# Kernel optimization log

Measured on AMD Instinct MI355X. Metric: run time of the kernel, lower is better.

The kernel has to match this reference:

```python
import jax, jax.numpy as jnp
import numpy as np


def setup_inputs() -> dict:
    key = jax.random.key(0)
    ks = jax.random.split(key, 7)
    B, T, Fin, H, O = 32, 2048, 256, 256, 256
    s = 1.0 / np.sqrt(H)
    return {
        "x":   jax.random.normal(ks[0], (B, T, Fin), dtype=jnp.float32),
        "h0":  jax.random.normal(ks[1], (B, H), dtype=jnp.float32),
        "Wxh": jax.random.normal(ks[2], (H, Fin), dtype=jnp.float32) * s,
        "bxh": jax.random.normal(ks[3], (H,), dtype=jnp.float32) * s,
        "Whh": jax.random.normal(ks[4], (H, H), dtype=jnp.float32) * s,
        "Why": jax.random.normal(ks[5], (O, H), dtype=jnp.float32) * s,
        "by":  jax.random.normal(ks[6], (O,), dtype=jnp.float32) * s,
    }


def reference(x, h0, Wxh, bxh, Whh, Why, by):
    # Batch the input projection across all T as one GEMM: (B,T,Fin)x(Fin,H)
    xh = jnp.einsum('btf,hf->bth', x, Wxh) + bxh  # (B,T,H)

    def step(h, xh_t):
        h = jnp.tanh(xh_t + h @ Whh.T)  # (B,H)
        return h, h

    # scan over time (axis 0 after transpose)
    h_final, hs = jax.lax.scan(step, h0, jnp.swapaxes(xh, 0, 1))  # hs: (T,B,H)
    hs = jnp.swapaxes(hs, 0, 1)  # (B,T,H)
    # Batch the output projection across all T as one GEMM
    y = jnp.einsum('bth,oh->bto', hs, Why) + by  # (B,T,O)
    return (y, h_final)
```

## Files before the change

kernel.cpp:

```cpp
#include <hip/hip_runtime.h>
#include <hip/hip_bf16.h>
#include <hip/hip_fp16.h>


typedef _Float16 f16x8 __attribute__((ext_vector_type(8)));
typedef float    f32x4 __attribute__((ext_vector_type(4)));

#define MFMA16 __builtin_amdgcn_mfma_f32_16x16x32_f16

__device__ __forceinline__ f16x8 cvt8(const float* __restrict__ p) {
    float4 u = *(const float4*)p;
    float4 v = *(const float4*)(p + 4);
    f16x8 r;
    r[0] = (_Float16)u.x; r[1] = (_Float16)u.y; r[2] = (_Float16)u.z; r[3] = (_Float16)u.w;
    r[4] = (_Float16)v.x; r[5] = (_Float16)v.y; r[6] = (_Float16)v.z; r[7] = (_Float16)v.w;
    return r;
}

template<bool AF16>
__global__ __launch_bounds__(256, 2) void gemm_nt_256(
    const void* __restrict__ Av, const float* __restrict__ W,
    const float* __restrict__ bias, float* __restrict__ C) {
    const int tid = threadIdx.x;
    const int l  = tid & 63;
    const int w  = tid >> 6;
    const int lr = l & 15;
    const int lg = l >> 4;
    const long m0 = (long)blockIdx.x * 64;
    const int  n0 = w * 64;

    f32x4 acc[4][4] = {};

    #pragma unroll
    for (int k = 0; k < 8; ++k) {
        const int kc = k * 32 + lg * 8;
        f16x8 a[4], bf[4];
        #pragma unroll
        for (int mt = 0; mt < 4; ++mt) {
            const long row = m0 + mt * 16 + lr;
            if constexpr (AF16)
                a[mt] = *(const f16x8*)((const _Float16*)Av + row * 256 + kc);
            else
                a[mt] = cvt8((const float*)Av + row * 256 + kc);
        }
        #pragma unroll
        for (int nt = 0; nt < 4; ++nt)
            bf[nt] = cvt8(W + (long)(n0 + nt * 16 + lr) * 256 + kc);
        #pragma unroll
        for (int mt = 0; mt < 4; ++mt)
            #pragma unroll
            for (int nt = 0; nt < 4; ++nt)
                acc[mt][nt] = MFMA16(a[mt], bf[nt], acc[mt][nt], 0, 0, 0);
    }

    #pragma unroll
    for (int mt = 0; mt < 4; ++mt)
        #pragma unroll
        for (int nt = 0; nt < 4; ++nt) {
            const int col = n0 + nt * 16 + lr;
            const float bv = bias[col];
            #pragma unroll
            for (int d = 0; d < 4; ++d) {
                const long row = m0 + mt * 16 + lg * 4 + d;
                C[row * 256 + col] = acc[mt][nt][d] + bv;
            }
        }
}

__global__ __launch_bounds__(512, 1) void rnn_scan(
    const float* __restrict__ xh, const float* __restrict__ h0,
    const float* __restrict__ Whh, _Float16* __restrict__ hs,
    float* __restrict__ hfin) {
    const int b   = blockIdx.x;
    const int tid = threadIdx.x;
    const int l   = tid & 63;
    const int w   = tid >> 6;
    const int lr  = l & 15;
    const int lg  = l >> 4;
    const int n0  = w * 32;

    __shared__ _Float16 hbuf[2][256];

    f16x8 wb[2][8];
    #pragma unroll
    for (int nt = 0; nt < 2; ++nt)
        #pragma unroll
        for (int k = 0; k < 8; ++k)
            wb[nt][k] = cvt8(Whh + (long)(n0 + nt * 16 + lr) * 256 + k * 32 + lg * 8);

    if (tid < 256) hbuf[0][tid] = (_Float16)h0[b * 256 + tid];
    __syncthreads();

    const int cl = n0 + (l & 31);
    const float* xp = xh + (long)b * 2048 * 256 + cl;
    _Float16*    hp = hs + (long)b * 2048 * 256 + cl;

    float xcur[4], xnext[4];
    #pragma unroll
    for (int j = 0; j < 4; ++j) xcur[j] = xp[(long)j * 256];

    for (int tb = 0; tb < 2048; tb += 4) {
        #pragma unroll
        for (int j = 0; j < 4; ++j) {
            long tn = tb + 4 + j; if (tn > 2047) tn = 2047;
            xnext[j] = xp[tn * 256];
        }

        #pragma unroll
        for (int j = 0; j < 4; ++j) {
            const f16x8* hc = (const f16x8*)hbuf[j & 1];
            f16x8 af[8];
            #pragma unroll
            for (int k = 0; k < 8; ++k) af[k] = hc[k * 4 + lg];
            __builtin_amdgcn_sched_barrier(0);

            const f32x4 zero = {0.f, 0.f, 0.f, 0.f};
            f32x4 accA[2], accB[2];
            #pragma unroll
            for (int nt = 0; nt < 2; ++nt) {
                accA[nt] = MFMA16(af[0], wb[nt][0], zero, 0, 0, 0);
                accB[nt] = MFMA16(af[4], wb[nt][4], zero, 0, 0, 0);
            }
            #pragma unroll
            for (int k = 1; k < 4; ++k)
                #pragma unroll
                for (int nt = 0; nt < 2; ++nt) {
                    accA[nt] = MFMA16(af[k],     wb[nt][k],     accA[nt], 0, 0, 0);
                    accB[nt] = MFMA16(af[k + 4], wb[nt][k + 4], accB[nt], 0, 0, 0);
                }

            const float s0 = accA[0][0] + accB[0][0];
            const float s1 = accA[1][0] + accB[1][0];
            const float s  = ((l & 16) ? s1 : s0) + xcur[j];
            const float e  = __expf(2.0f * s);
            const float v  = 1.0f - 2.0f * __builtin_amdgcn_rcpf(e + 1.0f);
            const _Float16 hv = (_Float16)v;

            if (l < 32) {
                hbuf[(j & 1) ^ 1][cl] = hv;
                hp[(long)(tb + j) * 256] = hv;
            }

            asm volatile("s_waitcnt lgkmcnt(0)" ::: "memory");
            __builtin_amdgcn_s_barrier();
            asm volatile("" ::: "memory");
        }

        #pragma unroll
        for (int j = 0; j < 4; ++j) xcur[j] = xnext[j];
    }

    if (tid < 256) hfin[b * 256 + tid] = (float)hbuf[0][tid];
}

extern "C" void kernel_launch(void* const* d_in, const int* in_sizes, int n_in,
                              void* d_out, int out_size, void* d_ws, size_t ws_size,
                              hipStream_t stream) {
    const float* x   = (const float*)d_in[0];
    const float* h0  = (const float*)d_in[1];
    const float* Wxh = (const float*)d_in[2];
    const float* bxh = (const float*)d_in[3];
    const float* Whh = (const float*)d_in[4];
    const float* Why = (const float*)d_in[5];
    const float* by  = (const float*)d_in[6];

    float* y    = (float*)d_out;
    float* hfin = y + (long)65536 * 256;
    float* xh   = y;
    _Float16* hs = (_Float16*)d_ws;

    gemm_nt_256<false><<<1024, 256, 0, stream>>>(x, Wxh, bxh, xh);
    rnn_scan<<<32, 512, 0, stream>>>(xh, h0, Whh, hs, hfin);
    gemm_nt_256<true><<<1024, 256, 0, stream>>>(hs, Why, by, y);
}
```

Before: 935.2 us.

## Replace per-step workgroup barrier with LDS flag spin-wait in RNN scan

The scan kernel no longer ends each timestep with s_barrier. Instead, each wave publishes its new slice of h to a double-buffered LDS array and raises a per-wave flag. Before reading the other slices, it spins on the eight flags using a ballot. Each wave's K order is rotated so it starts the MFMA on its own h slice before waiting, overlapping part of the serial recurrence with synchronisation. The cost is active spinning on volatile LDS reads, and correctness now depends on flag and buffer ordering rather than a hardware barrier.

Measured after the change: 1.112 ms. +18.9%, slower.

```diff
diff --git a/kernel.cpp b/kernel.cpp
--- a/kernel.cpp
+++ b/kernel.cpp
@@ -80,20 +80,26 @@
     const int n0  = w * 32;
 
     __shared__ _Float16 hbuf[2][256];
+    __shared__ unsigned flags[8];
 
-    f16x8 wb[2][8];
+    f16x8 wbr[2][8];
     #pragma unroll
-    for (int nt = 0; nt < 2; ++nt)
+    for (int i = 0; i < 8; ++i) {
+        const int k = (w + i) & 7;
         #pragma unroll
-        for (int k = 0; k < 8; ++k)
-            wb[nt][k] = cvt8(Whh + (long)(n0 + nt * 16 + lr) * 256 + k * 32 + lg * 8);
+        for (int nt = 0; nt < 2; ++nt)
+            wbr[nt][i] = cvt8(Whh + (long)(n0 + nt * 16 + lr) * 256 + k * 32 + lg * 8);
+    }
 
-    if (tid < 256) hbuf[0][tid] = (_Float16)h0[b * 256 + tid];
+    if (tid < 8) flags[tid] = 0;
     __syncthreads();
 
     const int cl = n0 + (l & 31);
     const float* xp = xh + (long)b * 2048 * 256 + cl;
     _Float16*    hp = hs + (long)b * 2048 * 256 + cl;
+    volatile unsigned* fl = flags;
+
+    _Float16 hv = (_Float16)h0[b * 256 + cl];
 
     float xcur[4], xnext[4];
     #pragma unroll
@@ -108,49 +114,54 @@
 
         #pragma unroll
         for (int j = 0; j < 4; ++j) {
-            const f16x8* hc = (const f16x8*)hbuf[j & 1];
-            f16x8 af[8];
-            #pragma unroll
-            for (int k = 0; k < 8; ++k) af[k] = hc[k * 4 + lg];
-            __builtin_amdgcn_sched_barrier(0);
+            const int t = tb + j;
+            _Float16* hb = hbuf[j & 1];
+            const f16x8* hc = (const f16x8*)hb;
+
+            if (l < 32) hb[cl] = hv;
+            asm volatile("s_waitcnt lgkmcnt(0)" ::: "memory");
+            if (l == 0) fl[w] = (unsigned)(t + 1);
+
+            f16x8 afr[8];
+            afr[0] = hc[(w & 7) * 4 + lg];
 
             const f32x4 zero = {0.f, 0.f, 0.f, 0.f};
             f32x4 accA[2], accB[2];
+            accA[0] = MFMA16(afr[0], wbr[0][0], zero, 0, 0, 0);
+            accA[1] = MFMA16(afr[0], wbr[1][0], zero, 0, 0, 0);
+
+            unsigned fv;
+            do { fv = fl[l & 7]; } while (__ballot(fv > (unsigned)t) != ~0ull);
+
             #pragma unroll
-            for (int nt = 0; nt < 2; ++nt) {
-                accA[nt] = MFMA16(af[0], wb[nt][0], zero, 0, 0, 0);
-                accB[nt] = MFMA16(af[4], wb[nt][4], zero, 0, 0, 0);
+            for (int i = 1; i < 8; ++i)
+                afr[i] = hc[((w + i) & 7) * 4 + lg];
+
+            accB[0] = MFMA16(afr[1], wbr[0][1], zero, 0, 0, 0);
+            accB[1] = MFMA16(afr[1], wbr[1][1], zero, 0, 0, 0);
+            #pragma unroll
+            for (int i = 2; i < 8; i += 2) {
+                accA[0] = MFMA16(afr[i],     wbr[0][i],     accA[0], 0, 0, 0);
+                accA[1] = MFMA16(afr[i],     wbr[1][i],     accA[1], 0, 0, 0);
+                accB[0] = MFMA16(afr[i + 1], wbr[0][i + 1], accB[0], 0, 0, 0);
+                accB[1] = MFMA16(afr[i + 1], wbr[1][i + 1], accB[1], 0, 0, 0);
             }
-            #pragma unroll
-            for (int k = 1; k < 4; ++k)
-                #pragma unroll
-                for (int nt = 0; nt < 2; ++nt) {
-                    accA[nt] = MFMA16(af[k],     wb[nt][k],     accA[nt], 0, 0, 0);
-                    accB[nt] = MFMA16(af[k + 4], wb[nt][k + 4], accB[nt], 0, 0, 0);
-                }
 
             const float s0 = accA[0][0] + accB[0][0];
             const float s1 = accA[1][0] + accB[1][0];
             const float s  = ((l & 16) ? s1 : s0) + xcur[j];
             const float e  = __expf(2.0f * s);
             const float v  = 1.0f - 2.0f * __builtin_amdgcn_rcpf(e + 1.0f);
-            const _Float16 hv = (_Float16)v;
+            hv = (_Float16)v;
 
-            if (l < 32) {
-                hbuf[(j & 1) ^ 1][cl] = hv;
-                hp[(long)(tb + j) * 256] = hv;
-            }
-
-            asm volatile("s_waitcnt lgkmcnt(0)" ::: "memory");
-            __builtin_amdgcn_s_barrier();
-            asm volatile("" ::: "memory");
+            if (l < 32) hp[(long)t * 256] = hv;
         }
 
         #pragma unroll
         for (int j = 0; j < 4; ++j) xcur[j] = xnext[j];
     }
 
-    if (tid < 256) hfin[b * 256 + tid] = (float)hbuf[0][tid];
+    if (l < 32) hfin[b * 256 + cl] = (float)hv;
 }
 
 extern "C" void kernel_launch(void* const* d_in, const int* in_sizes, int n_in,
```

## Replace MFMA recurrent matvec with per-lane scalar FMA dot products

Applied to the files above, without the earlier changes.

The recurrent step h@Whh^T in the scan kernel now uses plain FP32 FMAs instead of 16x16x32 MFMA tiles. Each lane holds half of one Whh row (128 fp16 values) in registers, reads the matching half of h from shared memory, and the two halves are combined with a cross-lane shuffle. The goal is to shorten the serial per-timestep latency: the old version ran a chain of dependent MFMAs per step and kept only one column of each 16x16 result. In exchange each lane does 128 scalar FMAs with fp16-to-fp32 conversions and reads 256 bytes of h from LDS per step. The final hidden state is now written in fp32 at the last step instead of being read back from the fp16 buffer.

Result: slower. 1.720 ms (+83.9%).

```diff
diff --git a/kernel.cpp b/kernel.cpp
--- a/kernel.cpp
+++ b/kernel.cpp
@@ -3,8 +3,8 @@
 #include <hip/hip_fp16.h>
 
 
-typedef _Float16 f16x8 __attribute__((ext_vector_type(8)));
-typedef float    f32x4 __attribute__((ext_vector_type(4)));
+typedef _Float16 f16x8  __attribute__((ext_vector_type(8)));
+typedef float    f32x4  __attribute__((ext_vector_type(4)));
 
 #define MFMA16 __builtin_amdgcn_mfma_f32_16x16x32_f16
 
@@ -71,29 +71,27 @@
     const float* __restrict__ xh, const float* __restrict__ h0,
     const float* __restrict__ Whh, _Float16* __restrict__ hs,
     float* __restrict__ hfin) {
-    const int b   = blockIdx.x;
-    const int tid = threadIdx.x;
-    const int l   = tid & 63;
-    const int w   = tid >> 6;
-    const int lr  = l & 15;
-    const int lg  = l >> 4;
-    const int n0  = w * 32;
+    const int b    = blockIdx.x;
+    const int tid  = threadIdx.x;
+    const int l    = tid & 63;
+    const int w    = tid >> 6;
+    const int col  = w * 32 + (l & 31);
+    const int half = l >> 5;
 
     __shared__ _Float16 hbuf[2][256];
 
-    f16x8 wb[2][8];
-    #pragma unroll
-    for (int nt = 0; nt < 2; ++nt)
+    f16x8 wreg8[16];
+    {
+        const float* wp = Whh + (long)col * 256 + half * 128;
         #pragma unroll
-        for (int k = 0; k < 8; ++k)
-            wb[nt][k] = cvt8(Whh + (long)(n0 + nt * 16 + lr) * 256 + k * 32 + lg * 8);
+        for (int i = 0; i < 16; ++i) wreg8[i] = cvt8(wp + 8 * i);
+    }
 
     if (tid < 256) hbuf[0][tid] = (_Float16)h0[b * 256 + tid];
     __syncthreads();
 
-    const int cl = n0 + (l & 31);
-    const float* xp = xh + (long)b * 2048 * 256 + cl;
-    _Float16*    hp = hs + (long)b * 2048 * 256 + cl;
+    const float* xp = xh + (long)b * 2048 * 256 + col;
+    _Float16*    hp = hs + (long)b * 2048 * 256 + col;
 
     float xcur[4], xnext[4];
     #pragma unroll
@@ -108,37 +106,40 @@
 
         #pragma unroll
         for (int j = 0; j < 4; ++j) {
-            const f16x8* hc = (const f16x8*)hbuf[j & 1];
-            f16x8 af[8];
+            const int t = tb + j;
+
+            const f16x8* hc = (const f16x8*)hbuf[j & 1] + half * 16;
+            f16x8 hreg[16];
             #pragma unroll
-            for (int k = 0; k < 8; ++k) af[k] = hc[k * 4 + lg];
-            __builtin_amdgcn_sched_barrier(0);
+            for (int i = 0; i < 16; ++i) hreg[i] = hc[i];
 
-            const f32x4 zero = {0.f, 0.f, 0.f, 0.f};
-            f32x4 accA[2], accB[2];
+            float s0 = 0.f, s1 = 0.f, s2 = 0.f, s3 = 0.f;
             #pragma unroll
-            for (int nt = 0; nt < 2; ++nt) {
-                accA[nt] = MFMA16(af[0], wb[nt][0], zero, 0, 0, 0);
-                accB[nt] = MFMA16(af[4], wb[nt][4], zero, 0, 0, 0);
+            for (int i = 0; i < 16; ++i) {
+                const f16x8 h8 = hreg[i];
+                const f16x8 w8 = wreg8[i];
+                s0 = fmaf((float)h8[0], (float)w8[0], s0);
+                s0 = fmaf((float)h8[1], (float)w8[1], s0);
+                s1 = fmaf((float)h8[2], (float)w8[2], s1);
+                s1 = fmaf((float)h8[3], (float)w8[3], s1);
+                s2 = fmaf((float)h8[4], (float)w8[4], s2);
+                s2 = fmaf((float)h8[5], (float)w8[5], s2);
+                s3 = fmaf((float)h8[6], (float)w8[6], s3);
+                s3 = fmaf((float)h8[7], (float)w8[7], s3);
             }
-            #pragma unroll
-            for (int k = 1; k < 4; ++k)
-                #pragma unroll
-                for (int nt = 0; nt < 2; ++nt) {
-                    accA[nt] = MFMA16(af[k],     wb[nt][k],     accA[nt], 0, 0, 0);
-                    accB[nt] = MFMA16(af[k + 4], wb[nt][k + 4], accB[nt], 0, 0, 0);
-                }
+            float s = (s0 + s1) + (s2 + s3);
 
-            const float s0 = accA[0][0] + accB[0][0];
-            const float s1 = accA[1][0] + accB[1][0];
-            const float s  = ((l & 16) ? s1 : s0) + xcur[j];
-            const float e  = __expf(2.0f * s);
+            s += __shfl_xor(s, 32, 64);
+
+            const float sx = s + xcur[j];
+            const float e  = __expf(2.0f * sx);
             const float v  = 1.0f - 2.0f * __builtin_amdgcn_rcpf(e + 1.0f);
             const _Float16 hv = (_Float16)v;
 
             if (l < 32) {
-                hbuf[(j & 1) ^ 1][cl] = hv;
-                hp[(long)(tb + j) * 256] = hv;
+                hbuf[(j & 1) ^ 1][col] = hv;
+                hp[(long)t * 256] = hv;
+                if (t == 2047) hfin[b * 256 + col] = v;
             }
 
             asm volatile("s_waitcnt lgkmcnt(0)" ::: "memory");
@@ -149,8 +150,6 @@
         #pragma unroll
         for (int j = 0; j < 4; ++j) xcur[j] = xnext[j];
     }
-
-    if (tid < 256) hfin[b * 256 + tid] = (float)hbuf[0][tid];
 }
 
 extern "C" void kernel_launch(void* const* d_in, const int* in_sizes, int n_in,
```

## Fuse input projection, recurrent scan and output projection into one kernel

Applied to the files above, without the earlier changes.

Replaces the three launches (input GEMM, scan, output GEMM) with a single 32-block kernel, one block per batch. Each block first computes its own input projection with Wxh held in registers. During the latency-bound scan it then interleaves output-projection MFMAs for 16-timestep tiles, lagging the recurrence by 8 tiles, and finishes the last tiles after the loop. The aim is to remove the separate GEMM launches and hide the output GEMM inside idle scan cycles. The cost is a serial prologue that now runs on only 32 CUs, with every wave re-reading the batch's x slab, plus extra register pressure during the scan.

Result: slower. 1.604 ms (+71.5%).

```diff
diff --git a/kernel.cpp b/kernel.cpp
--- a/kernel.cpp
+++ b/kernel.cpp
@@ -1,5 +1,4 @@
 #include <hip/hip_runtime.h>
-#include <hip/hip_bf16.h>
 #include <hip/hip_fp16.h>
 
 
@@ -17,60 +16,14 @@
     return r;
 }
 
-template<bool AF16>
-__global__ __launch_bounds__(256, 2) void gemm_nt_256(
-    const void* __restrict__ Av, const float* __restrict__ W,
-    const float* __restrict__ bias, float* __restrict__ C) {
-    const int tid = threadIdx.x;
-    const int l  = tid & 63;
-    const int w  = tid >> 6;
-    const int lr = l & 15;
-    const int lg = l >> 4;
-    const long m0 = (long)blockIdx.x * 64;
-    const int  n0 = w * 64;
-
-    f32x4 acc[4][4] = {};
-
-    #pragma unroll
-    for (int k = 0; k < 8; ++k) {
-        const int kc = k * 32 + lg * 8;
-        f16x8 a[4], bf[4];
-        #pragma unroll
-        for (int mt = 0; mt < 4; ++mt) {
-            const long row = m0 + mt * 16 + lr;
-            if constexpr (AF16)
-                a[mt] = *(const f16x8*)((const _Float16*)Av + row * 256 + kc);
-            else
-                a[mt] = cvt8((const float*)Av + row * 256 + kc);
-        }
-        #pragma unroll
-        for (int nt = 0; nt < 4; ++nt)
-            bf[nt] = cvt8(W + (long)(n0 + nt * 16 + lr) * 256 + kc);
-        #pragma unroll
-        for (int mt = 0; mt < 4; ++mt)
-            #pragma unroll
-            for (int nt = 0; nt < 4; ++nt)
-                acc[mt][nt] = MFMA16(a[mt], bf[nt], acc[mt][nt], 0, 0, 0);
-    }
-
-    #pragma unroll
-    for (int mt = 0; mt < 4; ++mt)
-        #pragma unroll
-        for (int nt = 0; nt < 4; ++nt) {
-            const int col = n0 + nt * 16 + lr;
-            const float bv = bias[col];
-            #pragma unroll
-            for (int d = 0; d < 4; ++d) {
-                const long row = m0 + mt * 16 + lg * 4 + d;
-                C[row * 256 + col] = acc[mt][nt][d] + bv;
-            }
-        }
-}
-
-__global__ __launch_bounds__(512, 1) void rnn_scan(
-    const float* __restrict__ xh, const float* __restrict__ h0,
-    const float* __restrict__ Whh, _Float16* __restrict__ hs,
-    float* __restrict__ hfin) {
+__global__ __launch_bounds__(512, 1) void rnn_fused(
+    const float* __restrict__ x,   const float* __restrict__ h0,
+    const float* __restrict__ Wxh, const float* __restrict__ bxh,
+    const float* __restrict__ Whh, const float* __restrict__ Why,
+    const float* __restrict__ by,
+    float* __restrict__ xy,
+    float* __restrict__ hfin,
+    _Float16* __restrict__ hs) {
     const int b   = blockIdx.x;
     const int tid = threadIdx.x;
     const int l   = tid & 63;
@@ -78,8 +31,13 @@
     const int lr  = l & 15;
     const int lg  = l >> 4;
     const int n0  = w * 32;
+    const int cl  = n0 + (l & 31);
 
     __shared__ _Float16 hbuf[2][256];
+
+    const float* xb  = x  + (long)b * 2048 * 256;
+    float*       xyb = xy + (long)b * 2048 * 256;
+    _Float16*    hpB = hs + (long)b * 2048 * 256;
 
     f16x8 wb[2][8];
     #pragma unroll
@@ -88,18 +46,78 @@
         for (int k = 0; k < 8; ++k)
             wb[nt][k] = cvt8(Whh + (long)(n0 + nt * 16 + lr) * 256 + k * 32 + lg * 8);
 
+    f16x8 wg[2][8];
+    #pragma unroll
+    for (int nt = 0; nt < 2; ++nt)
+        #pragma unroll
+        for (int k = 0; k < 8; ++k)
+            wg[nt][k] = cvt8(Wxh + (long)(n0 + nt * 16 + lr) * 256 + k * 32 + lg * 8);
+
     if (tid < 256) hbuf[0][tid] = (_Float16)h0[b * 256 + tid];
+
+    for (int mt = 0; mt < 128; ++mt) {
+        f32x4 ac[2] = {{0.f,0.f,0.f,0.f},{0.f,0.f,0.f,0.f}};
+        #pragma unroll
+        for (int k = 0; k < 8; ++k) {
+            const int kc = k * 32 + lg * 8;
+            f16x8 a = cvt8(xb + (long)(mt * 16 + lr) * 256 + kc);
+            ac[0] = MFMA16(a, wg[0][k], ac[0], 0, 0, 0);
+            ac[1] = MFMA16(a, wg[1][k], ac[1], 0, 0, 0);
+        }
+        #pragma unroll
+        for (int nt = 0; nt < 2; ++nt) {
+            const int col = n0 + nt * 16 + lr;
+            const float bv = bxh[col];
+            #pragma unroll
+            for (int d = 0; d < 4; ++d)
+                xyb[(long)(mt * 16 + lg * 4 + d) * 256 + col] = ac[nt][d] + bv;
+        }
+    }
+
+    #pragma unroll
+    for (int nt = 0; nt < 2; ++nt)
+        #pragma unroll
+        for (int k = 0; k < 8; ++k)
+            wg[nt][k] = cvt8(Why + (long)(n0 + nt * 16 + lr) * 256 + k * 32 + lg * 8);
+
     __syncthreads();
 
-    const int cl = n0 + (l & 31);
-    const float* xp = xh + (long)b * 2048 * 256 + cl;
-    _Float16*    hp = hs + (long)b * 2048 * 256 + cl;
+    const float* xp = xyb + cl;
+    _Float16*    hp = hpB + cl;
 
     float xcur[4], xnext[4];
     #pragma unroll
     for (int j = 0; j < 4; ++j) xcur[j] = xp[(long)j * 256];
 
+    f32x4 sacc[2] = {{0.f,0.f,0.f,0.f},{0.f,0.f,0.f,0.f}};
+    f16x8 pya[4];
+
+#define YS(P, K)                                               \
+    do {                                                       \
+        sacc[0] = MFMA16(pya[P], wg[0][K], sacc[0], 0, 0, 0);  \
+        sacc[1] = MFMA16(pya[P], wg[1][K], sacc[1], 0, 0, 0);  \
+    } while (0)
+
     for (int tb = 0; tb < 2048; tb += 4) {
+        const int g = tb >> 4;
+        const int m = g - 8;
+        const bool yact = (m >= 0) && (m <= 118);
+
+        if (yact && (tb & 15) == 0) {
+            const _Float16* ap = hpB + (long)(m * 16 + lr) * 256 + lg * 8;
+            pya[0] = *(const f16x8*)(ap);
+            pya[1] = *(const f16x8*)(ap + 32);
+            pya[2] = *(const f16x8*)(ap + 64);
+            pya[3] = *(const f16x8*)(ap + 96);
+        }
+        if (yact && (tb & 15) == 8) {
+            const _Float16* ap = hpB + (long)(m * 16 + lr) * 256 + 128 + lg * 8;
+            pya[0] = *(const f16x8*)(ap);
+            pya[1] = *(const f16x8*)(ap + 32);
+            pya[2] = *(const f16x8*)(ap + 64);
+            pya[3] = *(const f16x8*)(ap + 96);
+        }
+
         #pragma unroll
         for (int j = 0; j < 4; ++j) {
             long tn = tb + 4 + j; if (tn > 2047) tn = 2047;
@@ -108,6 +126,7 @@
 
         #pragma unroll
         for (int j = 0; j < 4; ++j) {
+            const int t = tb + j;
             const f16x8* hc = (const f16x8*)hbuf[j & 1];
             f16x8 af[8];
             #pragma unroll
@@ -138,7 +157,25 @@
 
             if (l < 32) {
                 hbuf[(j & 1) ^ 1][cl] = hv;
-                hp[(long)(tb + j) * 256] = hv;
+                hp[(long)t * 256] = hv;
+                if (t == 2047) hfin[b * 256 + cl] = v;
+            }
+
+            if (j == 1 && yact) {
+                switch ((tb >> 2) & 3) {
+                    case 0: YS(0, 0); break;
+                    case 1: YS(2, 2); break;
+                    case 2: YS(0, 4); break;
+                    case 3: YS(2, 6); break;
+                }
+            }
+            if (j == 3 && yact) {
+                switch ((tb >> 2) & 3) {
+                    case 0: YS(1, 1); break;
+                    case 1: YS(3, 3); break;
+                    case 2: YS(1, 5); break;
+                    case 3: YS(3, 7); break;
+                }
             }
 
             asm volatile("s_waitcnt lgkmcnt(0)" ::: "memory");
@@ -146,11 +183,42 @@
             asm volatile("" ::: "memory");
         }
 
+        if (yact && (tb & 15) == 12) {
+            #pragma unroll
+            for (int nt = 0; nt < 2; ++nt) {
+                const int col = n0 + nt * 16 + lr;
+                const float bv = by[col];
+                #pragma unroll
+                for (int d = 0; d < 4; ++d)
+                    xyb[(long)(m * 16 + lg * 4 + d) * 256 + col] = sacc[nt][d] + bv;
+                sacc[nt] = (f32x4){0.f, 0.f, 0.f, 0.f};
+            }
+        }
+
         #pragma unroll
         for (int j = 0; j < 4; ++j) xcur[j] = xnext[j];
     }
 
-    if (tid < 256) hfin[b * 256 + tid] = (float)hbuf[0][tid];
+    __syncthreads();
+    for (int mt = 119; mt < 128; ++mt) {
+        f32x4 ac[2] = {{0.f,0.f,0.f,0.f},{0.f,0.f,0.f,0.f}};
+        #pragma unroll
+        for (int k = 0; k < 8; ++k) {
+            const int kc = k * 32 + lg * 8;
+            f16x8 a = *(const f16x8*)(hpB + (long)(mt * 16 + lr) * 256 + kc);
+            ac[0] = MFMA16(a, wg[0][k], ac[0], 0, 0, 0);
+            ac[1] = MFMA16(a, wg[1][k], ac[1], 0, 0, 0);
+        }
+        #pragma unroll
+        for (int nt = 0; nt < 2; ++nt) {
+            const int col = n0 + nt * 16 + lr;
+            const float bv = by[col];
+            #pragma unroll
+            for (int d = 0; d < 4; ++d)
+                xyb[(long)(mt * 16 + lg * 4 + d) * 256 + col] = ac[nt][d] + bv;
+        }
+    }
+#undef YS
 }
 
 extern "C" void kernel_launch(void* const* d_in, const int* in_sizes, int n_in,
@@ -166,10 +234,7 @@
 
     float* y    = (float*)d_out;
     float* hfin = y + (long)65536 * 256;
-    float* xh   = y;
     _Float16* hs = (_Float16*)d_ws;
 
-    gemm_nt_256<false><<<1024, 256, 0, stream>>>(x, Wxh, bxh, xh);
-    rnn_scan<<<32, 512, 0, stream>>>(xh, h0, Whh, hs, hfin);
-    gemm_nt_256<true><<<1024, 256, 0, stream>>>(hs, Why, by, y);
+    rnn_fused<<<32, 512, 0, stream>>>(x, h0, Wxh, bxh, Whh, Why, by, y, hfin, hs);
 }
```
